# Kernel optimization log

Measured on AMD Instinct MI355X. Metric: run time of the kernel, lower is better.

## Reference

```python
import math
import jax, jax.numpy as jnp
import numpy as np

B, T, FDIM, ODIM = 16, 16, 64, 8
NQ, LAYERS, DEGREE = 10, 2, 3
NA = 4                      # ceil(log2(T))
TOT = NQ + NA               # 14 total wires
NROTS = 4 * NQ * LAYERS     # 80 params per timestep
QROTS = 4 * NQ              # 40 (qff circuit, 1 layer)
C64 = jnp.complex64


def ry_mat(t):
    c = jnp.cos(0.5 * t).astype(C64)
    s = jnp.sin(0.5 * t).astype(C64)
    return jnp.stack([jnp.stack([c, -s], -1), jnp.stack([s, c], -1)], -2)


def rz_mat(t):
    p = jnp.exp(-0.5j * t.astype(C64))
    q = jnp.exp(0.5j * t.astype(C64))
    z = jnp.zeros_like(p)
    return jnp.stack([jnp.stack([p, z], -1), jnp.stack([z, q], -1)], -2)


def crx_mat(t):
    c = jnp.cos(0.5 * t).astype(C64)
    s = (-1j) * jnp.sin(0.5 * t).astype(C64)
    z = jnp.zeros_like(c)
    o = jnp.ones_like(c)
    r0 = jnp.stack([o, z, z, z], -1)
    r1 = jnp.stack([z, o, z, z], -1)
    r2 = jnp.stack([z, z, c, s], -1)
    r3 = jnp.stack([z, z, s, c], -1)
    return jnp.stack([r0, r1, r2, r3], -2)


CNOT = jnp.array([[1, 0, 0, 0], [0, 1, 0, 0], [0, 0, 0, 1], [0, 0, 1, 0]], dtype=C64)


def apply_gate(state, U, wires):
    # state: (Be, 2,...,2) tensor; wire w lives on axis w+1. U: (2^k,2^k) or (Be,2^k,2^k)
    k = len(wires)
    axes = [w + 1 for w in wires]
    st = jnp.moveaxis(state, axes, list(range(1, k + 1)))
    shp = st.shape
    st = st.reshape(shp[0], 2 ** k, -1)
    eq = 'bij,bjr->bir' if U.ndim == 3 else 'ij,bjr->bir'
    st = jnp.einsum(eq, U, st).reshape(shp)
    return jnp.moveaxis(st, list(range(1, k + 1)), axes)


def sim14_seq(nq, layers):
    # gate sequence of Sim et al. circuit 14: RY ring, CRX ring, RY ring, CRX counter-ring
    seq, idx = [], 0
    for _ in range(layers):
        for i in range(nq):
            seq.append(('ry', (i,), idx)); idx += 1
        for i in range(nq - 1, -1, -1):
            seq.append(('crx', (i, (i + 1) % nq), idx)); idx += 1
        for i in range(nq):
            seq.append(('ry', (i,), idx)); idx += 1
        for i in [nq - 1] + list(range(nq - 1)):
            seq.append(('crx', (i, (i - 1) % nq), idx)); idx += 1
    return seq


def apply_sim14(state, params, layers, adjoint=False):
    seq = sim14_seq(NQ, layers)
    if adjoint:
        seq = seq[::-1]
    sign = -1.0 if adjoint else 1.0
    for kind, w, pidx in seq:
        th = sign * params[..., pidx]
        U = ry_mat(th) if kind == 'ry' else crx_mat(th)
        state = apply_gate(state, U, list(w))
    return state


def apply_prepare(state, prep_p, adjoint=False):
    # learnable PREPARE ansatz on ancilla wires NQ..NQ+NA-1 (n_prep_layers == NA)
    seq = []
    for ly in range(NA):
        for qi in range(NA):
            seq.append(('ry', NQ + qi, (ly, qi, 0)))
            seq.append(('rz', NQ + qi, (ly, qi, 1)))
        for i in range(NA - 1):
            seq.append(('cnot', (NQ + i, NQ + i + 1), None))
    if adjoint:
        seq = seq[::-1]
    sign = -1.0 if adjoint else 1.0
    for kind, w, pix in seq:
        if kind == 'cnot':
            state = apply_gate(state, CNOT, list(w))
        else:
            th = sign * prep_p[pix]
            U = ry_mat(th) if kind == 'ry' else rz_mat(th)
            state = apply_gate(state, U, [w])
    return state


def pcphase(state, phi):
    # PennyLane PCPhase(phi, dim=2^NQ, wires=anc+main): e^{+i phi} on ancilla==0 subspace, e^{-i phi} elsewhere
    st = state.reshape(B, 2 ** NQ, 2 ** NA)
    ph = jnp.exp(1j * phi.astype(C64))
    vec = jnp.where(jnp.arange(2 ** NA) == 0, ph, jnp.conj(ph))
    return (st * vec).reshape((B,) + (2,) * TOT)


def apply_select(state, ts_params, adjoint=False):
    # Select: apply sim14(ts_params[:, j]) on main wires when ancilla register == j
    # (T == 2^NA so there is no identity padding). Vectorized over batch x ancilla index.
    st = state.reshape(B, 2 ** NQ, 2 ** NA)
    st = jnp.moveaxis(st, 2, 1).reshape((B * T,) + (2,) * NQ)
    st = apply_sim14(st, ts_params.reshape(B * T, NROTS), LAYERS, adjoint)
    st = st.reshape(B, 2 ** NA, 2 ** NQ)
    return jnp.moveaxis(st, 1, 2).reshape((B,) + (2,) * TOT)


def expvals(state):
    # <X_i>, <Y_i>, <Z_i> on main wires, order X0..X9, Y0..Y9, Z0..Z9
    xs, ys, zs = [], [], []
    for i in range(NQ):
        s = jnp.moveaxis(state, i + 1, 1).reshape(B, 2, -1)
        s0, s1 = s[:, 0], s[:, 1]
        c = jnp.sum(jnp.conj(s0) * s1, axis=-1)
        xs.append(2.0 * jnp.real(c))
        ys.append(2.0 * jnp.imag(c))
        zs.append(jnp.sum(jnp.abs(s0) ** 2 - jnp.abs(s1) ** 2, axis=-1))
    return jnp.stack(xs + ys + zs, axis=1).astype(jnp.float32)  # (B, 3*NQ)


def make_pe():
    pos = np.arange(T, dtype=np.float32)[:, None]
    div = np.exp(np.arange(0, FDIM, 2, dtype=np.float32) * -(math.log(10000.0) / FDIM))
    pe = np.zeros((T, FDIM), np.float32)
    pe[:, 0::2] = np.sin(pos * div)
    pe[:, 1::2] = np.cos(pos * div[:FDIM // 2])
    return jnp.asarray(pe)


def setup_inputs():
    key = jax.random.key(0)
    ks = jax.random.split(key, 8)
    return {
        'x': jax.random.normal(ks[0], (B, FDIM, T), jnp.float32),
        'W_fp': jax.random.normal(ks[1], (NROTS, FDIM), jnp.float32) / math.sqrt(FDIM),
        'b_fp': jnp.zeros((NROTS,), jnp.float32),
        'prep_p': 0.1 * jax.random.normal(ks[2], (NA, NA, 2), jnp.float32),
        'sig_ang': 0.1 * jax.random.normal(ks[3], (DEGREE + 1,), jnp.float32),
        'qff_p': jax.random.uniform(ks[4], (QROTS,), jnp.float32),
        'W_out': jax.random.normal(ks[5], (ODIM, 3 * NQ), jnp.float32) / math.sqrt(3 * NQ),
        'b_out': jnp.zeros((ODIM,), jnp.float32),
    }


def reference(x, W_fp, b_fp, prep_p, sig_ang, qff_p, W_out, b_out):
    h = jnp.transpose(x, (0, 2, 1)) + make_pe()[None]          # (B, T, FDIM)
    ts = jax.nn.sigmoid(h @ W_fp.T + b_fp) * (2.0 * math.pi)    # (B, T, NROTS)
    # |0...0> on all 14 wires, batched
    psi = jnp.zeros((B, 2 ** TOT), C64).at[:, 0].set(1.0).reshape((B,) + (2,) * TOT)
    psi = pcphase(psi, sig_ang[0])
    for k in range(DEGREE):
        psi = apply_prepare(psi, prep_p, adjoint=False)
        psi = apply_select(psi, ts, adjoint=(k % 2 == 1))
        psi = apply_prepare(psi, prep_p, adjoint=True)
        psi = pcphase(psi, sig_ang[k + 1])
    psi = apply_sim14(psi, qff_p, layers=1, adjoint=False)      # QFF readout circuit
    exps = expvals(psi)                                         # (B, 30)
    return exps @ W_out.T + b_out                               # (B, ODIM)
```

## Files before the change

### kernel.cpp

```cpp
#include <hip/hip_runtime.h>
#include <math.h>
#include <utility>


typedef float v2f __attribute__((ext_vector_type(2)));

struct Gate { int ry; int tbit; int cbit; int pidx; };
struct GateTab { Gate g[40]; };

constexpr GateTab make_gates1() {
  GateTab tb{};
  int pos = 0, idx = 0;
  for (int i = 0; i < 10; ++i) { tb.g[pos] = Gate{1, 9 - i, -1, idx}; ++pos; ++idx; }
  for (int i = 9; i >= 0; --i) { tb.g[pos] = Gate{0, 9 - ((i + 1) % 10), 9 - i, idx}; ++pos; ++idx; }
  for (int i = 0; i < 10; ++i) { tb.g[pos] = Gate{1, 9 - i, -1, idx}; ++pos; ++idx; }
  for (int k = 0; k < 10; ++k) {
    int i = (k == 0) ? 9 : (k - 1);
    tb.g[pos] = Gate{0, 9 - ((i + 9) % 10), 9 - i, idx}; ++pos; ++idx;
  }
  return tb;
}
constexpr GateTab GTC = make_gates1();

__device__ __forceinline__ int insert_zero(int v, int p) {
  return ((v >> p) << (p + 1)) | (v & ((1 << p) - 1));
}
__device__ __forceinline__ float2 cmul(float2 A, float2 B) {
  return make_float2(A.x * B.x - A.y * B.y, A.x * B.y + A.y * B.x);
}
__device__ __forceinline__ float2 conj2(float2 A) { return make_float2(A.x, -A.y); }
__device__ __forceinline__ v2f vmk(float x, float y) { v2f r; r.x = x; r.y = y; return r; }

template<int XM>
__device__ __forceinline__ float lxor(float v) {
  if constexpr (XM == 1) {
    int r = __builtin_amdgcn_update_dpp(__float_as_int(v), __float_as_int(v),
                                        0xB1, 0xF, 0xF, true);
    return __int_as_float(r);
  } else if constexpr (XM == 2) {
    int r = __builtin_amdgcn_update_dpp(__float_as_int(v), __float_as_int(v),
                                        0x4E, 0xF, 0xF, true);
    return __int_as_float(r);
  } else if constexpr (XM == 8) {
    int r = __builtin_amdgcn_update_dpp(__float_as_int(v), __float_as_int(v),
                                        0x128, 0xF, 0xF, true);
    return __int_as_float(r);
  } else if constexpr (XM == 16) {
#if __has_builtin(__builtin_amdgcn_permlane16_swap)
    unsigned uv = __float_as_uint(v);
    auto r = __builtin_amdgcn_permlane16_swap(uv, uv, false, false);
    return __uint_as_float(r[0] ^ r[1] ^ uv);
#else
    return __shfl_xor(v, 16, 64);
#endif
  } else if constexpr (XM == 32) {
#if __has_builtin(__builtin_amdgcn_permlane32_swap)
    unsigned uv = __float_as_uint(v);
    auto r = __builtin_amdgcn_permlane32_swap(uv, uv, false, false);
    return __uint_as_float(r[0] ^ r[1] ^ uv);
#else
    return __shfl_xor(v, 32, 64);
#endif
  } else {
    return __shfl_xor(v, XM, 64);
  }
}
template<int XM>
__device__ __forceinline__ v2f lxor2(v2f v) {
  v2f r; r.x = lxor<XM>(v.x); r.y = lxor<XM>(v.y); return r;
}

__device__ __forceinline__ float wave_sum(float v) {
  v += lxor<1>(v);
  v += lxor<2>(v);
  v += lxor<4>(v);
  v += lxor<8>(v);
  v += lxor<16>(v);
  v += lxor<32>(v);
  return v;
}

struct alignas(128) GBar {
  unsigned cnt;
  unsigned gen;
  unsigned done;
  unsigned pad[29];
};
__device__ GBar g_gb[16];

__device__ __forceinline__ void group_barrier16(int b, int lane) {
  unsigned snap = __hip_atomic_load(&g_gb[b].gen, __ATOMIC_RELAXED, __HIP_MEMORY_SCOPE_AGENT);
  if (lane == 0) {
    unsigned old = __hip_atomic_fetch_add(&g_gb[b].cnt, 1u, __ATOMIC_ACQ_REL,
                                          __HIP_MEMORY_SCOPE_AGENT);
    if ((old & 15u) == 15u)
      __hip_atomic_store(&g_gb[b].gen, snap + 1u, __ATOMIC_RELEASE,
                         __HIP_MEMORY_SCOPE_AGENT);
  }
  while (__hip_atomic_load(&g_gb[b].gen, __ATOMIC_RELAXED, __HIP_MEMORY_SCOPE_AGENT) == snap)
    __builtin_amdgcn_s_sleep(1);
  (void)__hip_atomic_load(&g_gb[b].gen, __ATOMIC_ACQUIRE, __HIP_MEMORY_SCOPE_AGENT);
}

template<int P>
__device__ __forceinline__ void ry_gate(v2f (&a)[16], float c, float s, int lane) {
  if constexpr (P < 4) {
    constexpr int m = 1 << P;
#pragma unroll
    for (int r0 = 0; r0 < 16; ++r0) {
      if (!(r0 & m)) {
        int r1 = r0 | m;
        v2f a0 = a[r0], a1 = a[r1];
        a[r0] = c * a0 - s * a1;
        a[r1] = s * a0 + c * a1;
      }
    }
  } else {
    constexpr int xm = 1 << (P - 4);
    bool up = (lane >> (P - 4)) & 1;
    float sg = up ? s : -s;
#pragma unroll
    for (int r = 0; r < 16; ++r) {
      v2f wv = lxor2<xm>(a[r]);
      a[r] = c * a[r] + sg * wv;
    }
  }
}

template<int P, int Q>
__device__ __forceinline__ void crx_gate(v2f (&a)[16], float c, float s, int lane) {
  if constexpr (P < 4) {
    constexpr int m = 1 << P;
#pragma unroll
    for (int r0 = 0; r0 < 16; ++r0) {
      if (!(r0 & m)) {
        int r1 = r0 | m;
        bool act;
        if constexpr (Q < 4) act = (r0 >> Q) & 1;
        else act = (lane >> (Q - 4)) & 1;
        if (act) {
          v2f a0 = a[r0], a1 = a[r1];
          a[r0] = c * a0 + s * vmk(a1.y, -a1.x);
          a[r1] = c * a1 + s * vmk(a0.y, -a0.x);
        }
      }
    }
  } else {
    constexpr int xm = 1 << (P - 4);
#pragma unroll
    for (int r = 0; r < 16; ++r) {
      v2f wv = lxor2<xm>(a[r]);
      bool act;
      if constexpr (Q < 4) act = (r >> Q) & 1;
      else act = (lane >> (Q - 4)) & 1;
      if (act) a[r] = c * a[r] + s * vmk(wv.y, -wv.x);
    }
  }
}

template<bool ADJ, int G>
__device__ __forceinline__ void one_gate(v2f (&a)[16], const float2 (&sc)[40], int lane) {
  constexpr Gate g = GTC.g[ADJ ? (39 - G) : G];
  float2 scv = sc[g.pidx];
  float s = ADJ ? -scv.x : scv.x;
  float c = scv.y;
  if constexpr (g.ry != 0) ry_gate<g.tbit>(a, c, s, lane);
  else crx_gate<g.tbit, g.cbit>(a, c, s, lane);
}

template<bool ADJ, int... I>
__device__ __forceinline__ void run_layer_impl(v2f (&a)[16], const float2 (&sc)[40],
                                               int lane, std::integer_sequence<int, I...>) {
  (one_gate<ADJ, I>(a, sc, lane), ...);
}

template<bool ADJ>
__device__ __forceinline__ void run_layer(v2f (&a)[16], const float2* sc, int lane) {
  float2 rsc[40];
#pragma unroll
  for (int i = 0; i < 40; ++i) rsc[i] = sc[i];
  run_layer_impl<ADJ>(a, rsc, lane, std::make_integer_sequence<int, 40>{});
}

__global__ __launch_bounds__(256, 1) void k_fused(const float* __restrict__ x,
                                                  const float* __restrict__ W_fp,
                                                  const float* __restrict__ b_fp,
                                                  const float* __restrict__ prep,
                                                  const float* __restrict__ sig,
                                                  const float* __restrict__ qff,
                                                  const float* __restrict__ W_out,
                                                  const float* __restrict__ b_out,
                                                  float* __restrict__ out,
                                                  float4* __restrict__ part1,
                                                  float4* __restrict__ part2,
                                                  float* __restrict__ sv) {
  int blk = blockIdx.x;
  int b = blk >> 2, sub = blk & 3;
  int tid = threadIdx.x;
  int w = tid >> 6, lane = tid & 63;
  int aa = sub * 4 + w;

  __shared__ __align__(16) float h[4][64];
  __shared__ float2 scs[4][80];
  __shared__ float2 qscs[40];
  __shared__ float2 ps[32];
  __shared__ float2 es[4];
  __shared__ float2 u0s[16];
  __shared__ float4 R[2][512];

  if (sub == 0 && w == 0 && lane < 30) sv[b * 30 + lane] = 0.f;

  {
    int f = lane, k = f >> 1;
    float div = expf(-(float)(2 * k) * (logf(10000.f) / 64.f));
    float ang = (float)aa * div;
    float pe = (f & 1) ? cosf(ang) : sinf(ang);
    h[w][f] = x[(b * 64 + f) * 16 + aa] + pe;
  }
  if (w == 0) {
    if (lane < 32) {
      float s, c;
      sincosf(0.5f * prep[lane], &s, &c);
      ps[lane] = make_float2(s, c);
    } else if (lane < 36) {
      float s, c;
      sincosf(sig[lane - 32], &s, &c);
      es[lane - 32] = make_float2(c, s);
    }
  } else if (w == 1 && lane < 40) {
    float s, c;
    sincosf(0.5f * qff[lane], &s, &c);
    qscs[lane] = make_float2(s, c);
  }
  __syncthreads();

  if (w == 0) {
    float2 v[16];
#pragma unroll
    for (int i = 0; i < 16; ++i) v[i] = make_float2(i == 0 ? 1.f : 0.f, 0.f);
#pragma unroll 1
    for (int ly = 0; ly < 4; ++ly) {
#pragma unroll
      for (int qi = 0; qi < 4; ++qi) {
        int p = 3 - qi;
        float2 rc = ps[ly * 8 + qi * 2 + 0];
        {
          float s = rc.x, c = rc.y;
#pragma unroll
          for (int m = 0; m < 8; ++m) {
            int a0 = insert_zero(m, p), a1 = a0 | (1 << p);
            float2 t0 = v[a0], t1 = v[a1];
            v[a0] = make_float2(c * t0.x - s * t1.x, c * t0.y - s * t1.y);
            v[a1] = make_float2(s * t0.x + c * t1.x, s * t0.y + c * t1.y);
          }
        }
        rc = ps[ly * 8 + qi * 2 + 1];
        {
          float s = rc.x, c = rc.y;
#pragma unroll
          for (int m = 0; m < 8; ++m) {
            int a0 = insert_zero(m, p), a1 = a0 | (1 << p);
            float2 t0 = v[a0], t1 = v[a1];
            v[a0] = make_float2(c * t0.x + s * t0.y, c * t0.y - s * t0.x);
            v[a1] = make_float2(c * t1.x - s * t1.y, c * t1.y + s * t1.x);
          }
        }
      }
#pragma unroll
      for (int i = 0; i < 3; ++i) {
        int pc = 3 - i, pt = 2 - i;
#pragma unroll
        for (int m = 0; m < 4; ++m) {
          int mm = insert_zero(m, pt);
          mm = insert_zero(mm, pc);
          int a0 = mm | (1 << pc), a1 = a0 | (1 << pt);
          float2 t0 = v[a0], t1 = v[a1];
          v[a0] = t1; v[a1] = t0;
        }
      }
    }
    if (lane == 0) {
#pragma unroll
      for (int i = 0; i < 16; ++i) u0s[i] = v[i];
    }
  }

  {
    const float4* h4 = (const float4*)&h[w][0];
    for (int j = lane; j < 80; j += 64) {
      float acc = b_fp[j];
      const float4* w4 = (const float4*)(W_fp + j * 64);
#pragma unroll
      for (int k4 = 0; k4 < 16; ++k4) {
        float4 hh = h4[k4], ww = w4[k4];
        acc += hh.x * ww.x + hh.y * ww.y + hh.z * ww.z + hh.w * ww.w;
      }
      float sg = 1.f / (1.f + expf(-acc));
      float s, c;
      sincosf(sg * 3.14159265358979323846f, &s, &c);
      scs[w][j] = make_float2(s, c);
    }
  }
  __syncthreads();

  float2 u0aa = u0s[aa];
  float2 e0 = es[0], e1 = es[1], e2 = es[2];
  float2 m0  = cmul(u0aa, e0);
  float2 cu0 = conj2(u0aa);
  float2 ceA = conj2(e1);
  float2 wA  = make_float2(-2.f * e1.y * u0aa.y, 2.f * e1.y * u0aa.x);
  float2 ceB = conj2(e2);
  float2 wB  = make_float2(-2.f * e2.y * u0aa.y, 2.f * e2.y * u0aa.x);

  const float2* sc = &scs[w][0];
  v2f a[16];
#pragma unroll
  for (int r = 0; r < 16; ++r) a[r] = vmk(0.f, 0.f);
  if (lane == 0) a[0] = vmk(m0.x, m0.y);

#pragma unroll 1
  for (int ph = 0; ph < 7; ++ph) {
    if (ph == 2 || ph == 4) {
      float2 ce = (ph == 2) ? ceA : ceB;
      float2 wk = (ph == 2) ? wA : wB;
      float4* part = (ph == 2) ? part1 : part2;

      __syncthreads();
      if (w < 2) {
#pragma unroll
        for (int q = 0; q < 8; ++q) {
          float2 p0 = cmul(cu0, make_float2(a[2 * q].x, a[2 * q].y));
          float2 p1 = cmul(cu0, make_float2(a[2 * q + 1].x, a[2 * q + 1].y));
          R[w][q * 64 + lane] = make_float4(p0.x, p0.y, p1.x, p1.y);
        }
      }
      __syncthreads();
      if (w >= 2) {
#pragma unroll
        for (int q = 0; q < 8; ++q) {
          float4 v = R[w - 2][q * 64 + lane];
          float2 p0 = cmul(cu0, make_float2(a[2 * q].x, a[2 * q].y));
          float2 p1 = cmul(cu0, make_float2(a[2 * q + 1].x, a[2 * q + 1].y));
          R[w - 2][q * 64 + lane] =
              make_float4(v.x + p0.x, v.y + p0.y, v.z + p1.x, v.w + p1.y);
        }
      }
      __syncthreads();
#pragma unroll
      for (int qq = 0; qq < 2; ++qq) {
        int q = w * 2 + qq;
        float4 v0 = R[0][q * 64 + lane];
        float4 v1 = R[1][q * 64 + lane];
        part[(size_t)(b * 4 + sub) * 512 + q * 64 + lane] =
            make_float4(v0.x + v1.x, v0.y + v1.y, v0.z + v1.z, v0.w + v1.w);
      }
      group_barrier16(b, lane);

      float4 s4[8];
#pragma unroll
      for (int q = 0; q < 8; ++q) {
        float4 v0 = R[0][q * 64 + lane];
        float4 v1 = R[1][q * 64 + lane];
        s4[q] = make_float4(v0.x + v1.x, v0.y + v1.y, v0.z + v1.z, v0.w + v1.w);
      }
#pragma unroll 1
      for (int o = 1; o < 4; ++o) {
        int so = (sub + o) & 3;
        const float4* pp = part + (size_t)(b * 4 + so) * 512 + lane;
#pragma unroll
        for (int q = 0; q < 8; ++q) {
          float4 v = pp[q * 64];
          s4[q].x += v.x; s4[q].y += v.y; s4[q].z += v.z; s4[q].w += v.w;
        }
      }
#pragma unroll
      for (int q = 0; q < 8; ++q) {
        v2f a0 = a[2 * q], a1 = a[2 * q + 1];
        a[2 * q] = vmk(ce.x * a0.x - ce.y * a0.y + wk.x * s4[q].x - wk.y * s4[q].y,
                       ce.x * a0.y + ce.y * a0.x + wk.x * s4[q].y + wk.y * s4[q].x);
        a[2 * q + 1] = vmk(ce.x * a1.x - ce.y * a1.y + wk.x * s4[q].z - wk.y * s4[q].w,
                           ce.x * a1.y + ce.y * a1.x + wk.x * s4[q].w + wk.y * s4[q].z);
      }
    }
    const float2* scp;
    if (ph == 6) scp = &qscs[0];
    else scp = sc + ((ph == 1 || ph == 2 || ph == 5) ? 40 : 0);
    if (ph == 2 || ph == 3) run_layer<true>(a, scp, lane);
    else                    run_layer<false>(a, scp, lane);
  }

  {
    float obs[30];
#pragma unroll
    for (int p = 0; p <= 9; ++p) {
      int i = 9 - p;
      float cr = 0.f, ci = 0.f, zz = 0.f;
      if (p < 4) {
        int m = 1 << p;
#pragma unroll
        for (int r0 = 0; r0 < 16; ++r0) {
          if (!(r0 & m)) {
            v2f A0 = a[r0], A1 = a[r0 | m];
            cr += A0.x * A1.x + A0.y * A1.y;
            ci += A0.x * A1.y - A0.y * A1.x;
            zz += (A0.x * A0.x + A0.y * A0.y) - (A1.x * A1.x + A1.y * A1.y);
          }
        }
      } else {
        int xm = 1 << (p - 4);
        bool up = (lane >> (p - 4)) & 1;
#pragma unroll
        for (int r = 0; r < 16; ++r) {
          float wx = __shfl_xor(a[r].x, xm, 64);
          float wy = __shfl_xor(a[r].y, xm, 64);
          float n2 = a[r].x * a[r].x + a[r].y * a[r].y;
          if (!up) {
            cr += a[r].x * wx + a[r].y * wy;
            ci += a[r].x * wy - a[r].y * wx;
            zz += n2;
          } else {
            zz -= n2;
          }
        }
      }
      obs[i] = 2.f * cr;
      obs[10 + i] = 2.f * ci;
      obs[20 + i] = zz;
    }
#pragma unroll
    for (int j = 0; j < 30; ++j) obs[j] = wave_sum(obs[j]);

    float* Rf = (float*)R;
    __syncthreads();
    if (lane == 0) {
#pragma unroll
      for (int j = 0; j < 30; ++j) Rf[w * 30 + j] = obs[j];
    }
    __syncthreads();
    if (w == 0) {
      if (lane < 30) {
        float v = Rf[0 * 30 + lane] + Rf[1 * 30 + lane] +
                  Rf[2 * 30 + lane] + Rf[3 * 30 + lane];
        atomicAdd(&sv[b * 30 + lane], v);
      }
      int lastflag = 0;
      if (lane == 0) {
        unsigned old = __hip_atomic_fetch_add(&g_gb[b].done, 1u, __ATOMIC_ACQ_REL,
                                              __HIP_MEMORY_SCOPE_AGENT);
        lastflag = ((old & 3u) == 3u) ? 1 : 0;
      }
      lastflag = __shfl(lastflag, 0, 64);
      if (lastflag) {
        (void)__hip_atomic_load(&g_gb[b].done, __ATOMIC_ACQUIRE, __HIP_MEMORY_SCOPE_AGENT);
        if (lane < 8) {
          float acc = b_out[lane];
#pragma unroll
          for (int j = 0; j < 30; ++j) acc += W_out[lane * 30 + j] * sv[b * 30 + j];
          out[b * 8 + lane] = acc;
        }
      }
    }
  }
}

extern "C" void kernel_launch(void* const* d_in, const int* in_sizes, int n_in,
                              void* d_out, int out_size, void* d_ws, size_t ws_size,
                              hipStream_t stream) {
  const float* x     = (const float*)d_in[0];
  const float* W_fp  = (const float*)d_in[1];
  const float* b_fp  = (const float*)d_in[2];
  const float* prep  = (const float*)d_in[3];
  const float* sig   = (const float*)d_in[4];
  const float* qff   = (const float*)d_in[5];
  const float* W_out = (const float*)d_in[6];
  const float* b_out = (const float*)d_in[7];
  float* out = (float*)d_out;
  (void)in_sizes; (void)n_in; (void)out_size;

  char* ws = (char*)d_ws;
  const size_t SZ_PART = (size_t)64 * 512 * 16;
  float4* part1 = (float4*)ws;
  float4* part2 = (float4*)(ws + SZ_PART);
  float*  sv    = (float*)(ws + 2 * SZ_PART);
  (void)ws_size;

  k_fused<<<dim3(64), dim3(256), 0, stream>>>(x, W_fp, b_fp, prep, sig, qff,
                                              W_out, b_out, out, part1, part2, sv);
}
```

Before: 163.5 us.

## Process one batch per block with four ancilla columns per wave, drop global barriers

Changes the work split from four blocks per batch element, each wave holding one ancilla column, to one block per batch element where each wave holds four ancilla columns in registers. The select-phase reduction over ancilla columns now happens entirely in shared memory within the block. This removes the cross-block spin barrier, global partial buffers and the atomic final reduction. It also adds a ds_swizzle path for the lane-xor-4 exchange. In exchange only 16 blocks run and each thread does four times the gate arithmetic with four times the register state, which risks spills and low occupancy.

```diff
diff --git a/kernel.cpp b/kernel.cpp
--- a/kernel.cpp
+++ b/kernel.cpp
@@ -40,6 +40,9 @@
   } else if constexpr (XM == 2) {
     int r = __builtin_amdgcn_update_dpp(__float_as_int(v), __float_as_int(v),
                                         0x4E, 0xF, 0xF, true);
+    return __int_as_float(r);
+  } else if constexpr (XM == 4) {
+    int r = __builtin_amdgcn_ds_swizzle(__float_as_int(v), 0x101F);
     return __int_as_float(r);
   } else if constexpr (XM == 8) {
     int r = __builtin_amdgcn_update_dpp(__float_as_int(v), __float_as_int(v),
@@ -53,7 +56,7 @@
 #else
     return __shfl_xor(v, 16, 64);
 #endif
-  } else if constexpr (XM == 32) {
+  } else {
 #if __has_builtin(__builtin_amdgcn_permlane32_swap)
     unsigned uv = __float_as_uint(v);
     auto r = __builtin_amdgcn_permlane32_swap(uv, uv, false, false);
@@ -61,8 +64,6 @@
 #else
     return __shfl_xor(v, 32, 64);
 #endif
-  } else {
-    return __shfl_xor(v, XM, 64);
   }
 }
 template<int XM>
@@ -80,106 +81,102 @@
   return v;
 }
 
-struct alignas(128) GBar {
-  unsigned cnt;
-  unsigned gen;
-  unsigned done;
-  unsigned pad[29];
-};
-__device__ GBar g_gb[16];
-
-__device__ __forceinline__ void group_barrier16(int b, int lane) {
-  unsigned snap = __hip_atomic_load(&g_gb[b].gen, __ATOMIC_RELAXED, __HIP_MEMORY_SCOPE_AGENT);
-  if (lane == 0) {
-    unsigned old = __hip_atomic_fetch_add(&g_gb[b].cnt, 1u, __ATOMIC_ACQ_REL,
-                                          __HIP_MEMORY_SCOPE_AGENT);
-    if ((old & 15u) == 15u)
-      __hip_atomic_store(&g_gb[b].gen, snap + 1u, __ATOMIC_RELEASE,
-                         __HIP_MEMORY_SCOPE_AGENT);
-  }
-  while (__hip_atomic_load(&g_gb[b].gen, __ATOMIC_RELAXED, __HIP_MEMORY_SCOPE_AGENT) == snap)
-    __builtin_amdgcn_s_sleep(1);
-  (void)__hip_atomic_load(&g_gb[b].gen, __ATOMIC_ACQUIRE, __HIP_MEMORY_SCOPE_AGENT);
-}
-
 template<int P>
-__device__ __forceinline__ void ry_gate(v2f (&a)[16], float c, float s, int lane) {
+__device__ __forceinline__ void ry_gate(v2f (&a)[4][16], const float (&c)[4],
+                                        const float (&s)[4], int lane) {
   if constexpr (P < 4) {
     constexpr int m = 1 << P;
 #pragma unroll
-    for (int r0 = 0; r0 < 16; ++r0) {
-      if (!(r0 & m)) {
-        int r1 = r0 | m;
-        v2f a0 = a[r0], a1 = a[r1];
-        a[r0] = c * a0 - s * a1;
-        a[r1] = s * a0 + c * a1;
+    for (int col = 0; col < 4; ++col) {
+      float cc = c[col], ss = s[col];
+#pragma unroll
+      for (int r0 = 0; r0 < 16; ++r0) {
+        if (!(r0 & m)) {
+          int r1 = r0 | m;
+          v2f a0 = a[col][r0], a1 = a[col][r1];
+          a[col][r0] = cc * a0 - ss * a1;
+          a[col][r1] = ss * a0 + cc * a1;
+        }
       }
     }
   } else {
     constexpr int xm = 1 << (P - 4);
     bool up = (lane >> (P - 4)) & 1;
-    float sg = up ? s : -s;
-#pragma unroll
-    for (int r = 0; r < 16; ++r) {
-      v2f wv = lxor2<xm>(a[r]);
-      a[r] = c * a[r] + sg * wv;
+#pragma unroll
+    for (int col = 0; col < 4; ++col) {
+      float cc = c[col];
+      float sg = up ? s[col] : -s[col];
+#pragma unroll
+      for (int r = 0; r < 16; ++r) {
+        v2f wv = lxor2<xm>(a[col][r]);
+        a[col][r] = cc * a[col][r] + sg * wv;
+      }
     }
   }
 }
 
 template<int P, int Q>
-__device__ __forceinline__ void crx_gate(v2f (&a)[16], float c, float s, int lane) {
+__device__ __forceinline__ void crx_gate(v2f (&a)[4][16], const float (&c)[4],
+                                         const float (&s)[4], int lane) {
   if constexpr (P < 4) {
     constexpr int m = 1 << P;
 #pragma unroll
-    for (int r0 = 0; r0 < 16; ++r0) {
-      if (!(r0 & m)) {
-        int r1 = r0 | m;
-        bool act;
-        if constexpr (Q < 4) act = (r0 >> Q) & 1;
-        else act = (lane >> (Q - 4)) & 1;
-        if (act) {
-          v2f a0 = a[r0], a1 = a[r1];
-          a[r0] = c * a0 + s * vmk(a1.y, -a1.x);
-          a[r1] = c * a1 + s * vmk(a0.y, -a0.x);
+    for (int col = 0; col < 4; ++col) {
+      float cc = c[col], ss = s[col];
+#pragma unroll
+      for (int r0 = 0; r0 < 16; ++r0) {
+        if (!(r0 & m)) {
+          int r1 = r0 | m;
+          bool act;
+          if constexpr (Q < 4) act = (r0 >> Q) & 1;
+          else act = (lane >> (Q - 4)) & 1;
+          if (act) {
+            v2f a0 = a[col][r0], a1 = a[col][r1];
+            a[col][r0] = cc * a0 + ss * vmk(a1.y, -a1.x);
+            a[col][r1] = cc * a1 + ss * vmk(a0.y, -a0.x);
+          }
         }
       }
     }
   } else {
     constexpr int xm = 1 << (P - 4);
 #pragma unroll
-    for (int r = 0; r < 16; ++r) {
-      v2f wv = lxor2<xm>(a[r]);
-      bool act;
-      if constexpr (Q < 4) act = (r >> Q) & 1;
-      else act = (lane >> (Q - 4)) & 1;
-      if (act) a[r] = c * a[r] + s * vmk(wv.y, -wv.x);
-    }
-  }
-}
-
-template<bool ADJ, int G>
-__device__ __forceinline__ void one_gate(v2f (&a)[16], const float2 (&sc)[40], int lane) {
+    for (int col = 0; col < 4; ++col) {
+      float cc = c[col], ss = s[col];
+#pragma unroll
+      for (int r = 0; r < 16; ++r) {
+        v2f wv = lxor2<xm>(a[col][r]);
+        bool act;
+        if constexpr (Q < 4) act = (r >> Q) & 1;
+        else act = (lane >> (Q - 4)) & 1;
+        if (act) a[col][r] = cc * a[col][r] + ss * vmk(wv.y, -wv.x);
+      }
+    }
+  }
+}
+
+template<bool ADJ, int CSTRIDE, int G>
+__device__ __forceinline__ void one_gate(v2f (&a)[4][16], const float2* sc, int lane) {
   constexpr Gate g = GTC.g[ADJ ? (39 - G) : G];
-  float2 scv = sc[g.pidx];
-  float s = ADJ ? -scv.x : scv.x;
-  float c = scv.y;
+  float c[4], s[4];
+#pragma unroll
+  for (int col = 0; col < 4; ++col) {
+    float2 scv = sc[col * CSTRIDE + g.pidx];
+    s[col] = ADJ ? -scv.x : scv.x;
+    c[col] = scv.y;
+  }
   if constexpr (g.ry != 0) ry_gate<g.tbit>(a, c, s, lane);
   else crx_gate<g.tbit, g.cbit>(a, c, s, lane);
 }
 
-template<bool ADJ, int... I>
-__device__ __forceinline__ void run_layer_impl(v2f (&a)[16], const float2 (&sc)[40],
+template<bool ADJ, int CSTRIDE, int... I>
+__device__ __forceinline__ void run_layer_impl(v2f (&a)[4][16], const float2* sc,
                                                int lane, std::integer_sequence<int, I...>) {
-  (one_gate<ADJ, I>(a, sc, lane), ...);
-}
-
-template<bool ADJ>
-__device__ __forceinline__ void run_layer(v2f (&a)[16], const float2* sc, int lane) {
-  float2 rsc[40];
-#pragma unroll
-  for (int i = 0; i < 40; ++i) rsc[i] = sc[i];
-  run_layer_impl<ADJ>(a, rsc, lane, std::make_integer_sequence<int, 40>{});
+  (one_gate<ADJ, CSTRIDE, I>(a, sc, lane), ...);
+}
+template<bool ADJ, int CSTRIDE>
+__device__ __forceinline__ void run_layer(v2f (&a)[4][16], const float2* sc, int lane) {
+  run_layer_impl<ADJ, CSTRIDE>(a, sc, lane, std::make_integer_sequence<int, 40>{});
 }
 
 __global__ __launch_bounds__(256, 1) void k_fused(const float* __restrict__ x,
@@ -190,47 +187,40 @@
                                                   const float* __restrict__ qff,
                                                   const float* __restrict__ W_out,
                                                   const float* __restrict__ b_out,
-                                                  float* __restrict__ out,
-                                                  float4* __restrict__ part1,
-                                                  float4* __restrict__ part2,
-                                                  float* __restrict__ sv) {
-  int blk = blockIdx.x;
-  int b = blk >> 2, sub = blk & 3;
+                                                  float* __restrict__ out) {
+  int b = blockIdx.x;
   int tid = threadIdx.x;
   int w = tid >> 6, lane = tid & 63;
-  int aa = sub * 4 + w;
-
-  __shared__ __align__(16) float h[4][64];
-  __shared__ float2 scs[4][80];
+
+  __shared__ float2 R[4][1024];
+  __shared__ __align__(16) float h[16][64];
+  __shared__ float2 scs[16][80];
   __shared__ float2 qscs[40];
   __shared__ float2 ps[32];
   __shared__ float2 es[4];
   __shared__ float2 u0s[16];
-  __shared__ float4 R[2][512];
-
-  if (sub == 0 && w == 0 && lane < 30) sv[b * 30 + lane] = 0.f;
-
-  {
-    int f = lane, k = f >> 1;
+
+  for (int i = tid; i < 1024; i += 256) {
+    int cc = i >> 6, f = i & 63, k = f >> 1;
     float div = expf(-(float)(2 * k) * (logf(10000.f) / 64.f));
-    float ang = (float)aa * div;
+    float ang = (float)cc * div;
     float pe = (f & 1) ? cosf(ang) : sinf(ang);
-    h[w][f] = x[(b * 64 + f) * 16 + aa] + pe;
-  }
-  if (w == 0) {
+    h[cc][f] = x[(b * 64 + f) * 16 + cc] + pe;
+  }
+  if (w == 1) {
     if (lane < 32) {
-      float s, c;
-      sincosf(0.5f * prep[lane], &s, &c);
-      ps[lane] = make_float2(s, c);
+      float s, cc;
+      sincosf(0.5f * prep[lane], &s, &cc);
+      ps[lane] = make_float2(s, cc);
     } else if (lane < 36) {
-      float s, c;
-      sincosf(sig[lane - 32], &s, &c);
-      es[lane - 32] = make_float2(c, s);
-    }
-  } else if (w == 1 && lane < 40) {
-    float s, c;
-    sincosf(0.5f * qff[lane], &s, &c);
-    qscs[lane] = make_float2(s, c);
+      float s, cc;
+      sincosf(sig[lane - 32], &s, &cc);
+      es[lane - 32] = make_float2(cc, s);
+    }
+  } else if (w == 2 && lane < 40) {
+    float s, cc;
+    sincosf(0.5f * qff[lane], &s, &cc);
+    qscs[lane] = make_float2(s, cc);
   }
   __syncthreads();
 
@@ -245,24 +235,24 @@
         int p = 3 - qi;
         float2 rc = ps[ly * 8 + qi * 2 + 0];
         {
-          float s = rc.x, c = rc.y;
+          float s = rc.x, cc = rc.y;
 #pragma unroll
           for (int m = 0; m < 8; ++m) {
             int a0 = insert_zero(m, p), a1 = a0 | (1 << p);
             float2 t0 = v[a0], t1 = v[a1];
-            v[a0] = make_float2(c * t0.x - s * t1.x, c * t0.y - s * t1.y);
-            v[a1] = make_float2(s * t0.x + c * t1.x, s * t0.y + c * t1.y);
+            v[a0] = make_float2(cc * t0.x - s * t1.x, cc * t0.y - s * t1.y);
+            v[a1] = make_float2(s * t0.x + cc * t1.x, s * t0.y + cc * t1.y);
           }
         }
         rc = ps[ly * 8 + qi * 2 + 1];
         {
-          float s = rc.x, c = rc.y;
+          float s = rc.x, cc = rc.y;
 #pragma unroll
           for (int m = 0; m < 8; ++m) {
             int a0 = insert_zero(m, p), a1 = a0 | (1 << p);
             float2 t0 = v[a0], t1 = v[a1];
-            v[a0] = make_float2(c * t0.x + s * t0.y, c * t0.y - s * t0.x);
-            v[a1] = make_float2(c * t1.x - s * t1.y, c * t1.y + s * t1.x);
+            v[a0] = make_float2(cc * t0.x + s * t0.y, cc * t0.y - s * t0.x);
+            v[a1] = make_float2(cc * t1.x - s * t1.y, cc * t1.y + s * t1.x);
           }
         }
       }
@@ -285,8 +275,10 @@
     }
   }
 
-  {
-    const float4* h4 = (const float4*)&h[w][0];
+#pragma unroll 1
+  for (int col = 0; col < 4; ++col) {
+    int cc = w * 4 + col;
+    const float4* h4 = (const float4*)&h[cc][0];
     for (int j = lane; j < 80; j += 64) {
       float acc = b_fp[j];
       const float4* w4 = (const float4*)(W_fp + j * 64);
@@ -296,97 +288,73 @@
         acc += hh.x * ww.x + hh.y * ww.y + hh.z * ww.z + hh.w * ww.w;
       }
       float sg = 1.f / (1.f + expf(-acc));
-      float s, c;
-      sincosf(sg * 3.14159265358979323846f, &s, &c);
-      scs[w][j] = make_float2(s, c);
+      float s, cfv;
+      sincosf(sg * 3.14159265358979323846f, &s, &cfv);
+      scs[cc][j] = make_float2(s, cfv);
     }
   }
   __syncthreads();
 
-  float2 u0aa = u0s[aa];
   float2 e0 = es[0], e1 = es[1], e2 = es[2];
-  float2 m0  = cmul(u0aa, e0);
-  float2 cu0 = conj2(u0aa);
-  float2 ceA = conj2(e1);
-  float2 wA  = make_float2(-2.f * e1.y * u0aa.y, 2.f * e1.y * u0aa.x);
-  float2 ceB = conj2(e2);
-  float2 wB  = make_float2(-2.f * e2.y * u0aa.y, 2.f * e2.y * u0aa.x);
-
-  const float2* sc = &scs[w][0];
-  v2f a[16];
-#pragma unroll
-  for (int r = 0; r < 16; ++r) a[r] = vmk(0.f, 0.f);
-  if (lane == 0) a[0] = vmk(m0.x, m0.y);
+  float2 u0c[4], m0c[4];
+#pragma unroll
+  for (int col = 0; col < 4; ++col) {
+    u0c[col] = u0s[w * 4 + col];
+    m0c[col] = cmul(u0c[col], e0);
+  }
+  float2 ceA = conj2(e1), ceB = conj2(e2);
+
+  const float2* sc = &scs[w * 4][0];
+  v2f a[4][16];
+#pragma unroll
+  for (int col = 0; col < 4; ++col) {
+#pragma unroll
+    for (int r = 0; r < 16; ++r) a[col][r] = vmk(0.f, 0.f);
+    if (lane == 0) a[col][0] = vmk(m0c[col].x, m0c[col].y);
+  }
 
 #pragma unroll 1
   for (int ph = 0; ph < 7; ++ph) {
     if (ph == 2 || ph == 4) {
       float2 ce = (ph == 2) ? ceA : ceB;
-      float2 wk = (ph == 2) ? wA : wB;
-      float4* part = (ph == 2) ? part1 : part2;
+      float ey = (ph == 2) ? e1.y : e2.y;
 
       __syncthreads();
-      if (w < 2) {
-#pragma unroll
-        for (int q = 0; q < 8; ++q) {
-          float2 p0 = cmul(cu0, make_float2(a[2 * q].x, a[2 * q].y));
-          float2 p1 = cmul(cu0, make_float2(a[2 * q + 1].x, a[2 * q + 1].y));
-          R[w][q * 64 + lane] = make_float4(p0.x, p0.y, p1.x, p1.y);
-        }
+#pragma unroll
+      for (int r = 0; r < 16; ++r) {
+        float px = 0.f, py = 0.f;
+#pragma unroll
+        for (int col = 0; col < 4; ++col) {
+          float2 cu = conj2(u0c[col]);
+          v2f ar = a[col][r];
+          px += cu.x * ar.x - cu.y * ar.y;
+          py += cu.x * ar.y + cu.y * ar.x;
+        }
+        R[w][r * 64 + lane] = make_float2(px, py);
       }
       __syncthreads();
-      if (w >= 2) {
-#pragma unroll
-        for (int q = 0; q < 8; ++q) {
-          float4 v = R[w - 2][q * 64 + lane];
-          float2 p0 = cmul(cu0, make_float2(a[2 * q].x, a[2 * q].y));
-          float2 p1 = cmul(cu0, make_float2(a[2 * q + 1].x, a[2 * q + 1].y));
-          R[w - 2][q * 64 + lane] =
-              make_float4(v.x + p0.x, v.y + p0.y, v.z + p1.x, v.w + p1.y);
-        }
-      }
-      __syncthreads();
-#pragma unroll
-      for (int qq = 0; qq < 2; ++qq) {
-        int q = w * 2 + qq;
-        float4 v0 = R[0][q * 64 + lane];
-        float4 v1 = R[1][q * 64 + lane];
-        part[(size_t)(b * 4 + sub) * 512 + q * 64 + lane] =
-            make_float4(v0.x + v1.x, v0.y + v1.y, v0.z + v1.z, v0.w + v1.w);
-      }
-      group_barrier16(b, lane);
-
-      float4 s4[8];
-#pragma unroll
-      for (int q = 0; q < 8; ++q) {
-        float4 v0 = R[0][q * 64 + lane];
-        float4 v1 = R[1][q * 64 + lane];
-        s4[q] = make_float4(v0.x + v1.x, v0.y + v1.y, v0.z + v1.z, v0.w + v1.w);
-      }
-#pragma unroll 1
-      for (int o = 1; o < 4; ++o) {
-        int so = (sub + o) & 3;
-        const float4* pp = part + (size_t)(b * 4 + so) * 512 + lane;
-#pragma unroll
-        for (int q = 0; q < 8; ++q) {
-          float4 v = pp[q * 64];
-          s4[q].x += v.x; s4[q].y += v.y; s4[q].z += v.z; s4[q].w += v.w;
-        }
-      }
-#pragma unroll
-      for (int q = 0; q < 8; ++q) {
-        v2f a0 = a[2 * q], a1 = a[2 * q + 1];
-        a[2 * q] = vmk(ce.x * a0.x - ce.y * a0.y + wk.x * s4[q].x - wk.y * s4[q].y,
-                       ce.x * a0.y + ce.y * a0.x + wk.x * s4[q].y + wk.y * s4[q].x);
-        a[2 * q + 1] = vmk(ce.x * a1.x - ce.y * a1.y + wk.x * s4[q].z - wk.y * s4[q].w,
-                           ce.x * a1.y + ce.y * a1.x + wk.x * s4[q].w + wk.y * s4[q].z);
-      }
-    }
-    const float2* scp;
-    if (ph == 6) scp = &qscs[0];
-    else scp = sc + ((ph == 1 || ph == 2 || ph == 5) ? 40 : 0);
-    if (ph == 2 || ph == 3) run_layer<true>(a, scp, lane);
-    else                    run_layer<false>(a, scp, lane);
+      float2 s2[16];
+#pragma unroll
+      for (int r = 0; r < 16; ++r) {
+        float2 v0 = R[0][r * 64 + lane], v1 = R[1][r * 64 + lane];
+        float2 v2 = R[2][r * 64 + lane], v3 = R[3][r * 64 + lane];
+        s2[r] = make_float2(v0.x + v1.x + v2.x + v3.x, v0.y + v1.y + v2.y + v3.y);
+      }
+#pragma unroll
+      for (int col = 0; col < 4; ++col) {
+        float2 wk = make_float2(-2.f * ey * u0c[col].y, 2.f * ey * u0c[col].x);
+#pragma unroll
+        for (int r = 0; r < 16; ++r) {
+          v2f a0 = a[col][r];
+          a[col][r] = vmk(ce.x * a0.x - ce.y * a0.y + wk.x * s2[r].x - wk.y * s2[r].y,
+                          ce.x * a0.y + ce.y * a0.x + wk.x * s2[r].y + wk.y * s2[r].x);
+        }
+      }
+    }
+    if (ph == 2)      run_layer<true, 80>(a, sc + 40, lane);
+    else if (ph == 3) run_layer<true, 80>(a, sc, lane);
+    else if (ph == 6) run_layer<false, 0>(a, &qscs[0], lane);
+    else              run_layer<false, 80>(a, sc + ((ph == 1 || ph == 5) ? 40 : 0), lane);
   }
 
   {
@@ -398,28 +366,34 @@
       if (p < 4) {
         int m = 1 << p;
 #pragma unroll
-        for (int r0 = 0; r0 < 16; ++r0) {
-          if (!(r0 & m)) {
-            v2f A0 = a[r0], A1 = a[r0 | m];
-            cr += A0.x * A1.x + A0.y * A1.y;
-            ci += A0.x * A1.y - A0.y * A1.x;
-            zz += (A0.x * A0.x + A0.y * A0.y) - (A1.x * A1.x + A1.y * A1.y);
+        for (int col = 0; col < 4; ++col) {
+#pragma unroll
+          for (int r0 = 0; r0 < 16; ++r0) {
+            if (!(r0 & m)) {
+              v2f A0 = a[col][r0], A1 = a[col][r0 | m];
+              cr += A0.x * A1.x + A0.y * A1.y;
+              ci += A0.x * A1.y - A0.y * A1.x;
+              zz += (A0.x * A0.x + A0.y * A0.y) - (A1.x * A1.x + A1.y * A1.y);
+            }
           }
         }
       } else {
         int xm = 1 << (p - 4);
         bool up = (lane >> (p - 4)) & 1;
 #pragma unroll
-        for (int r = 0; r < 16; ++r) {
-          float wx = __shfl_xor(a[r].x, xm, 64);
-          float wy = __shfl_xor(a[r].y, xm, 64);
-          float n2 = a[r].x * a[r].x + a[r].y * a[r].y;
-          if (!up) {
-            cr += a[r].x * wx + a[r].y * wy;
-            ci += a[r].x * wy - a[r].y * wx;
-            zz += n2;
-          } else {
-            zz -= n2;
+        for (int col = 0; col < 4; ++col) {
+#pragma unroll
+          for (int r = 0; r < 16; ++r) {
+            float wx = __shfl_xor(a[col][r].x, xm, 64);
+            float wy = __shfl_xor(a[col][r].y, xm, 64);
+            float n2 = a[col][r].x * a[col][r].x + a[col][r].y * a[col][r].y;
+            if (!up) {
+              cr += a[col][r].x * wx + a[col][r].y * wy;
+              ci += a[col][r].x * wy - a[col][r].y * wx;
+              zz += n2;
+            } else {
+              zz -= n2;
+            }
           }
         }
       }
@@ -430,35 +404,21 @@
 #pragma unroll
     for (int j = 0; j < 30; ++j) obs[j] = wave_sum(obs[j]);
 
-    float* Rf = (float*)R;
+    float* Rf = (float*)&R[0][0];
     __syncthreads();
     if (lane == 0) {
 #pragma unroll
       for (int j = 0; j < 30; ++j) Rf[w * 30 + j] = obs[j];
     }
     __syncthreads();
-    if (w == 0) {
-      if (lane < 30) {
-        float v = Rf[0 * 30 + lane] + Rf[1 * 30 + lane] +
-                  Rf[2 * 30 + lane] + Rf[3 * 30 + lane];
-        atomicAdd(&sv[b * 30 + lane], v);
-      }
-      int lastflag = 0;
-      if (lane == 0) {
-        unsigned old = __hip_atomic_fetch_add(&g_gb[b].done, 1u, __ATOMIC_ACQ_REL,
-                                              __HIP_MEMORY_SCOPE_AGENT);
-        lastflag = ((old & 3u) == 3u) ? 1 : 0;
-      }
-      lastflag = __shfl(lastflag, 0, 64);
-      if (lastflag) {
-        (void)__hip_atomic_load(&g_gb[b].done, __ATOMIC_ACQUIRE, __HIP_MEMORY_SCOPE_AGENT);
-        if (lane < 8) {
-          float acc = b_out[lane];
-#pragma unroll
-          for (int j = 0; j < 30; ++j) acc += W_out[lane * 30 + j] * sv[b * 30 + j];
-          out[b * 8 + lane] = acc;
-        }
-      }
+    if (w == 0 && lane < 8) {
+      float acc = b_out[lane];
+#pragma unroll
+      for (int j = 0; j < 30; ++j) {
+        float svj = Rf[0 * 30 + j] + Rf[1 * 30 + j] + Rf[2 * 30 + j] + Rf[3 * 30 + j];
+        acc += W_out[lane * 30 + j] * svj;
+      }
+      out[b * 8 + lane] = acc;
     }
   }
 }
@@ -475,15 +435,8 @@
   const float* W_out = (const float*)d_in[6];
   const float* b_out = (const float*)d_in[7];
   float* out = (float*)d_out;
-  (void)in_sizes; (void)n_in; (void)out_size;
-
-  char* ws = (char*)d_ws;
-  const size_t SZ_PART = (size_t)64 * 512 * 16;
-  float4* part1 = (float4*)ws;
-  float4* part2 = (float4*)(ws + SZ_PART);
-  float*  sv    = (float*)(ws + 2 * SZ_PART);
-  (void)ws_size;
-
-  k_fused<<<dim3(64), dim3(256), 0, stream>>>(x, W_fp, b_fp, prep, sig, qff,
-                                              W_out, b_out, out, part1, part2, sv);
-}
+  (void)d_ws; (void)ws_size; (void)in_sizes; (void)n_in; (void)out_size;
+
+  k_fused<<<dim3(16), dim3(256), 0, stream>>>(x, W_fp, b_fp, prep, sig, qff,
+                                              W_out, b_out, out);
+}
```

New measurement: 411.4 us. 152% more time.
